# Kernel optimization log

Hardware: AMD Instinct MI355X
Metric: run time of the kernel (lower is better)

Reference implementation:

```python
import jax, jax.numpy as jnp
import numpy as np
from jax import lax

PATCH = 32  # enc conv kernel/stride
EPS = 1e-12  # F.normalize eps


def setup_inputs() -> dict:
    key = jax.random.key(0)
    ks = jax.random.split(key, 7)
    B, N, H, W = 32, 256, 32, 32
    fdim, vdim = 512, 128
    x = jax.random.normal(ks[0], (B, 3 * N, H, W), dtype=jnp.float32)
    conv_w = jax.random.normal(ks[1], (fdim, 3, PATCH, PATCH), dtype=jnp.float32) * (1.0 / np.sqrt(3 * PATCH * PATCH))
    conv_b = jax.random.normal(ks[2], (fdim,), dtype=jnp.float32) * 0.01
    fc1_w = jax.random.normal(ks[3], (vdim, fdim), dtype=jnp.float32) * (1.0 / np.sqrt(fdim))
    fc1_b = jax.random.normal(ks[4], (vdim,), dtype=jnp.float32) * 0.01
    # deterministic dropout masks (p=0.5, train mode -> keep * 1/(1-p))
    drop1 = (jax.random.uniform(ks[5], (B, N, N)) >= 0.5).astype(jnp.float32) * 2.0
    drop2 = (jax.random.uniform(ks[6], (B, N, N)) >= 0.5).astype(jnp.float32) * 2.0
    return {"x": x, "conv_w": conv_w, "conv_b": conv_b,
            "fc1_w": fc1_w, "fc1_b": fc1_b, "drop1": drop1, "drop2": drop2}


def _branch(scores, drop, eye):
    # softmax over dim=-2, zero diag, dropout, L1-normalize over dim=-2
    P = jax.nn.softmax(scores, axis=-2)
    P = P * (1.0 - eye)
    P = P * drop
    denom = jnp.maximum(jnp.sum(jnp.abs(P), axis=-2, keepdims=True), EPS)
    return P / denom


def reference(x, conv_w, conv_b, fc1_w, fc1_b, drop1, drop2):
    B, C, H, W = x.shape
    N = C // 3
    xi = x.reshape(B * N, 3, H, W)
    # enc: patchify conv -> (B*N, fdim, 1, 1)
    fm = lax.conv_general_dilated(xi, conv_w, (PATCH, PATCH), 'VALID',
                                  dimension_numbers=('NCHW', 'OIHW', 'NCHW'))
    fm = fm + conv_b[None, :, None, None]
    # map2vec: adaptive avgpool(1,1) + flatten + fc1
    v = fm.mean(axis=(2, 3))                      # (B*N, fdim)
    v = v @ fc1_w.T + fc1_b                       # (B*N, vdim)
    f = v.reshape(B, N, -1)                       # (B, N, vdim)
    f_norm = f / jnp.maximum(jnp.linalg.norm(f, axis=-1, keepdims=True), EPS)
    A = jnp.einsum('bnd,bmd->bnm', f_norm, f_norm)  # cosine affinity (B,N,N)
    Atemp = A * (128.0 ** 0.5)                    # torch.div(A, 1/128**0.5)
    eye = jnp.eye(N, dtype=A.dtype)
    A1 = _branch(Atemp, drop1, eye)
    A2t = _branch(jnp.swapaxes(Atemp, -1, -2), drop2, eye)
    AtA = jnp.swapaxes(jnp.matmul(A2t, A1), -1, -2)
    # nll_loss(AtA, arange targets) == -mean of diagonal entries
    diag = jnp.einsum('bii->bi', AtA)
    loss = -jnp.mean(diag)
    return f, A, loss
```

## Files before the change

kernel.cpp:

```cpp
#include <hip/hip_runtime.h>
#include <stdint.h>

#define S_SCALE 11.313708498984761f
#define EPS 1e-12f

typedef __bf16 bf16x8 __attribute__((ext_vector_type(8)));
typedef float  f32x4  __attribute__((ext_vector_type(4)));

__device__ __forceinline__ f32x4 mfma16(bf16x8 a, bf16x8 b, f32x4 c) {
  return __builtin_amdgcn_mfma_f32_16x16x32_bf16(a, b, c, 0, 0, 0);
}

__device__ __forceinline__ float waveSum(float v) {
#pragma unroll
  for (int m = 32; m > 0; m >>= 1) v += __shfl_xor(v, m, 64);
  return v;
}

__device__ __forceinline__ void load_lds16(const float* g, float* l) {
  __builtin_amdgcn_global_load_lds(
      (const __attribute__((address_space(1))) uint32_t*)g,
      (__attribute__((address_space(3))) uint32_t*)l, 16, 0, 0);
}

#define OFF_W    0
#define OFF_BIAS 786432
#define OFF_FN   786944
#define OFF_ZP   2884096
#define OFF_P1   3146240

__global__ __launch_bounds__(256) void k_prep(const float* __restrict__ conv_w,
                                              const float* __restrict__ fc1_w,
                                              const float* __restrict__ conv_b,
                                              const float* __restrict__ fc1_b,
                                              __bf16* __restrict__ W,
                                              float* __restrict__ bias2,
                                              float* __restrict__ loss) {
  __shared__ float cw_s[64][36];
  __shared__ float fc1_s[128][65];
  __shared__ float red[4];
  const int t = threadIdx.x;
  if (blockIdx.x >= 96) {
    const int o = blockIdx.x - 96;
    if (o == 0 && t == 0) loss[0] = 0.f;
    float p = fc1_w[o * 512 + t] * conv_b[t] +
              fc1_w[o * 512 + 256 + t] * conv_b[256 + t];
    p = waveSum(p);
    if ((t & 63) == 0) red[t >> 6] = p;
    __syncthreads();
    if (t == 0) bias2[o] = red[0] + red[1] + red[2] + red[3] + fc1_b[o];
    return;
  }
  const int kt = blockIdx.x;
  const int k0 = kt * 32;
  const int og = t >> 3, kg = t & 7;
  float acc[4][4] = {};
  for (int cs = 0; cs < 8; ++cs) {
    const int cc = cs * 64;
    __syncthreads();
#pragma unroll
    for (int i = 0; i < 8; ++i) {
      int idx = t + 256 * i;
      int cr = idx >> 5, kk = idx & 31;
      cw_s[cr][kk] = conv_w[(cc + cr) * 3072 + k0 + kk];
    }
#pragma unroll
    for (int i = 0; i < 8; ++i) {
      int idx = t + 256 * i;
      int o = idx >> 4, c4 = (idx & 15) * 4;
      float4 v = *(const float4*)&fc1_w[o * 512 + cc + c4];
      fc1_s[o][c4 + 0] = v.x; fc1_s[o][c4 + 1] = v.y;
      fc1_s[o][c4 + 2] = v.z; fc1_s[o][c4 + 3] = v.w;
    }
    __syncthreads();
    for (int ci = 0; ci < 64; ++ci) {
      float4 cw = *(const float4*)&cw_s[ci][kg * 4];
#pragma unroll
      for (int j = 0; j < 4; ++j) {
        float fv = fc1_s[og * 4 + j][ci];
        acc[j][0] = fmaf(fv, cw.x, acc[j][0]);
        acc[j][1] = fmaf(fv, cw.y, acc[j][1]);
        acc[j][2] = fmaf(fv, cw.z, acc[j][2]);
        acc[j][3] = fmaf(fv, cw.w, acc[j][3]);
      }
    }
  }
#pragma unroll
  for (int j = 0; j < 4; ++j)
#pragma unroll
    for (int q = 0; q < 4; ++q)
      W[(og * 4 + j) * 3072 + k0 + kg * 4 + q] = (__bf16)acc[j][q];
}

__device__ __forceinline__ void stageA(const float* __restrict__ x,
                                       float* __restrict__ lds, int wave,
                                       const int dr[2], const int dc[2],
                                       int m0, int k0) {
#pragma unroll
  for (int j = 0; j < 2; ++j)
    load_lds16(x + (m0 + dr[j]) * 3072 + k0 + dc[j],
               lds + (wave * 2 + j) * 256);
}

__device__ __forceinline__ void loadB(const __bf16* __restrict__ bp, int k0,
                                      uint4 (&dst)[2][2]) {
#pragma unroll
  for (int ks = 0; ks < 2; ++ks)
#pragma unroll
    for (int ni = 0; ni < 2; ++ni)
      dst[ks][ni] = *(const uint4*)(bp + ni * 16 * 3072 + k0 + ks * 32);
}

__device__ __forceinline__ void computeTile(const float* __restrict__ Abuf,
                                            const uint4 (&breg)[2][2],
                                            int l15, int quad,
                                            f32x4 (&acc)[2][2]) {
#pragma unroll
  for (int ks = 0; ks < 2; ++ks) {
    bf16x8 afrag[2];
#pragma unroll
    for (int mi = 0; mi < 2; ++mi) {
      const int rb = (l15 + mi * 16) * 64;
      float4 lo = *(const float4*)&Abuf[rb + (((ks * 8 + quad * 2 + 0) ^ l15) << 2)];
      float4 hi = *(const float4*)&Abuf[rb + (((ks * 8 + quad * 2 + 1) ^ l15) << 2)];
      union { __bf16 h[8]; bf16x8 v; } pk;
      pk.h[0] = (__bf16)lo.x; pk.h[1] = (__bf16)lo.y;
      pk.h[2] = (__bf16)lo.z; pk.h[3] = (__bf16)lo.w;
      pk.h[4] = (__bf16)hi.x; pk.h[5] = (__bf16)hi.y;
      pk.h[6] = (__bf16)hi.z; pk.h[7] = (__bf16)hi.w;
      afrag[mi] = pk.v;
    }
#pragma unroll
    for (int mi = 0; mi < 2; ++mi)
#pragma unroll
      for (int ni = 0; ni < 2; ++ni)
        acc[mi][ni] = mfma16(afrag[mi], *(const bf16x8*)&breg[ks][ni],
                             acc[mi][ni]);
  }
}

__global__ __launch_bounds__(256) void k_gemm1(const float* __restrict__ x,
                                               const __bf16* __restrict__ W,
                                               float* __restrict__ P0,
                                               float* __restrict__ P1) {
  __shared__ __align__(16) float A_lds[2][32 * 64];
  const int t = threadIdx.x;
  const int wave = t >> 6, lane = t & 63;
  const int l15 = lane & 15, quad = lane >> 4;
  const int m0 = blockIdx.x * 32;
  const int kbase = blockIdx.y * 1536;
  float* P = blockIdx.y ? P1 : P0;

  int dr[2], dc[2];
#pragma unroll
  for (int j = 0; j < 2; ++j) {
    int row = wave * 8 + j * 4 + (lane >> 4);
    int cl = (lane & 15) ^ (row & 15);
    dr[j] = row;
    dc[j] = cl * 4;
  }

  f32x4 acc[2][2] = {{{0.f,0.f,0.f,0.f},{0.f,0.f,0.f,0.f}},
                     {{0.f,0.f,0.f,0.f},{0.f,0.f,0.f,0.f}}};
  const __bf16* bp = W + (wave * 32 + l15) * 3072 + quad * 8;

  uint4 bA[2][2], bB[2][2];
  stageA(x, &A_lds[0][0], wave, dr, dc, m0, kbase);
  loadB(bp, kbase, bA);
  __syncthreads();

  for (int it2 = 0; it2 < 12; ++it2) {
    const int itA = it2 * 2;
    stageA(x, &A_lds[1][0], wave, dr, dc, m0, kbase + (itA + 1) * 64);
    loadB(bp, kbase + (itA + 1) * 64, bB);
    __builtin_amdgcn_sched_barrier(0);
    computeTile(&A_lds[0][0], bA, l15, quad, acc);
    __syncthreads();
    if (it2 < 11) {
      stageA(x, &A_lds[0][0], wave, dr, dc, m0, kbase + (itA + 2) * 64);
      loadB(bp, kbase + (itA + 2) * 64, bA);
    }
    __builtin_amdgcn_sched_barrier(0);
    computeTile(&A_lds[1][0], bB, l15, quad, acc);
    __syncthreads();
  }

#pragma unroll
  for (int mi = 0; mi < 2; ++mi)
#pragma unroll
    for (int ni = 0; ni < 2; ++ni) {
      int col = wave * 32 + ni * 16 + l15;
#pragma unroll
      for (int r = 0; r < 4; ++r) {
        int row = m0 + mi * 16 + quad * 4 + r;
        P[row * 128 + col] = acc[mi][ni][r];
      }
    }
}

__global__ __launch_bounds__(256) void k_fin(float* __restrict__ f_inout,
                                             const float* __restrict__ P1,
                                             const float* __restrict__ bias2,
                                             __bf16* __restrict__ fn) {
  const int wave = threadIdx.x >> 6, lane = threadIdx.x & 63;
  const int row = blockIdx.x * 4 + wave;
  const int i0 = row * 128 + lane, i1 = i0 + 64;
  float v0 = f_inout[i0] + P1[i0] + bias2[lane];
  float v1 = f_inout[i1] + P1[i1] + bias2[lane + 64];
  float ss = waveSum(fmaf(v0, v0, v1 * v1));
  float inv = 1.f / fmaxf(sqrtf(ss), EPS);
  f_inout[i0] = v0;
  f_inout[i1] = v1;
  fn[i0] = (__bf16)(v0 * inv);
  fn[i1] = (__bf16)(v1 * inv);
}

__global__ __launch_bounds__(256) void k_gemm2(const __bf16* __restrict__ fn,
                                               const float* __restrict__ d1,
                                               const float* __restrict__ d2,
                                               float* __restrict__ Aout,
                                               float* __restrict__ Zp) {
  __shared__ __align__(16) __bf16 Li[64][136];
  __shared__ __align__(16) __bf16 Lj[64][136];
  __shared__ float zred[2][4][64];
  const int t = threadIdx.x;
  const int b = blockIdx.y;
  const int ti = blockIdx.x >> 2, tj = blockIdx.x & 3;
  const int i0 = ti * 64, j0 = tj * 64;
  const int wave = t >> 6, lane = t & 63;
  const int l15 = lane & 15, quad = lane >> 4;
  const __bf16* fb = fn + b * 32768;
#pragma unroll
  for (int i = 0; i < 4; ++i) {
    int idx = t + 256 * i;
    int r = idx >> 4, c8 = (idx & 15) * 8;
    *(uint4*)&Li[r][c8] = *(const uint4*)&fb[(i0 + r) * 128 + c8];
    *(uint4*)&Lj[r][c8] = *(const uint4*)&fb[(j0 + r) * 128 + c8];
  }
  __syncthreads();
  f32x4 acc[4] = {{0.f, 0.f, 0.f, 0.f}, {0.f, 0.f, 0.f, 0.f},
                  {0.f, 0.f, 0.f, 0.f}, {0.f, 0.f, 0.f, 0.f}};
#pragma unroll
  for (int ks = 0; ks < 4; ++ks) {
    bf16x8 af = *(const bf16x8*)&Li[wave * 16 + l15][ks * 32 + quad * 8];
#pragma unroll
    for (int nt = 0; nt < 4; ++nt) {
      bf16x8 bf = *(const bf16x8*)&Lj[nt * 16 + l15][ks * 32 + quad * 8];
      acc[nt] = mfma16(af, bf, acc[nt]);
    }
  }
  const int base = b * 65536;
  float* Ab = Aout + base;
  float z1c[4] = {0.f, 0.f, 0.f, 0.f}, z2c[4] = {0.f, 0.f, 0.f, 0.f};
#pragma unroll
  for (int nt = 0; nt < 4; ++nt) {
    int gj = j0 + nt * 16 + l15;
#pragma unroll
    for (int r = 0; r < 4; ++r) {
      int gi = i0 + wave * 16 + quad * 4 + r;
      float a = acc[nt][r];
      Ab[gi * 256 + gj] = a;
      float e = __expf(fmaf(S_SCALE, a, -S_SCALE));
      if (gi != gj) {
        int idx = base + gi * 256 + gj;
        z1c[nt] = fmaf(e, d1[idx], z1c[nt]);
        z2c[nt] = fmaf(e, d2[idx], z2c[nt]);
      }
    }
  }
#pragma unroll
  for (int nt = 0; nt < 4; ++nt) {
    z1c[nt] += __shfl_xor(z1c[nt], 16, 64);
    z1c[nt] += __shfl_xor(z1c[nt], 32, 64);
    z2c[nt] += __shfl_xor(z2c[nt], 16, 64);
    z2c[nt] += __shfl_xor(z2c[nt], 32, 64);
  }
  if (quad == 0) {
#pragma unroll
    for (int nt = 0; nt < 4; ++nt) {
      zred[0][wave][nt * 16 + l15] = z1c[nt];
      zred[1][wave][nt * 16 + l15] = z2c[nt];
    }
  }
  __syncthreads();
  if (t < 128) {
    int z = t >> 6, c = t & 63;
    float s = zred[z][0][c] + zred[z][1][c] + zred[z][2][c] + zred[z][3][c];
    Zp[(z * 4 + ti) * 8192 + b * 256 + j0 + c] = s;
  }
}

__global__ __launch_bounds__(256) void k_loss(const float* __restrict__ Aout,
                                              const float* __restrict__ d1,
                                              const float* __restrict__ d2,
                                              const float* __restrict__ Zp,
                                              float* __restrict__ loss) {
  __shared__ float d1s[64][65];
  __shared__ float z1s[64], z2s[64];
  __shared__ float red[4];
  const int t = threadIdx.x;
  const int b = blockIdx.y;
  const int ic = blockIdx.x >> 2, kc = blockIdx.x & 3;
  const int i0 = ic * 64, k0 = kc * 64;
  const int base = b * 65536;
  if (t < 64) {
    float s = 0.f;
#pragma unroll
    for (int p = 0; p < 4; ++p) s += Zp[p * 8192 + b * 256 + i0 + t];
    z1s[t] = 1.f / fmaxf(s, EPS);
  } else if (t < 128) {
    float s = 0.f;
#pragma unroll
    for (int p = 0; p < 4; ++p) s += Zp[(4 + p) * 8192 + b * 256 + k0 + t - 64];
    z2s[t - 64] = 1.f / fmaxf(s, EPS);
  }
#pragma unroll
  for (int ii = 0; ii < 16; ++ii) {
    int idx = t + 256 * ii;
    int kr = idx >> 6, ci = idx & 63;
    d1s[kr][ci] = d1[base + (k0 + kr) * 256 + i0 + ci];
  }
  __syncthreads();
  const int kl = t & 63, ig = t >> 6;
  float inv2 = z2s[kl];
  float accv = 0.f;
  for (int ii = 0; ii < 16; ++ii) {
    int il = ig * 16 + ii;
    int idx = base + (i0 + il) * 256 + k0 + kl;
    float a = Aout[idx];
    float e = __expf(fmaf(2.f * S_SCALE, a, -2.f * S_SCALE));
    float v = e * d2[idx] * d1s[kl][il] * z1s[il] * inv2;
    if (i0 + il != k0 + kl) accv += v;
  }
  accv = waveSum(accv);
  if ((t & 63) == 0) red[t >> 6] = accv;
  __syncthreads();
  if (t == 0) {
    float tot = red[0] + red[1] + red[2] + red[3];
    atomicAdd(loss, tot * (-1.f / 8192.f));
  }
}

extern "C" void kernel_launch(void* const* d_in, const int* in_sizes, int n_in,
                              void* d_out, int out_size, void* d_ws,
                              size_t ws_size, hipStream_t stream) {
  const float* x = (const float*)d_in[0];
  const float* conv_w = (const float*)d_in[1];
  const float* conv_b = (const float*)d_in[2];
  const float* fc1_w = (const float*)d_in[3];
  const float* fc1_b = (const float*)d_in[4];
  const float* drop1 = (const float*)d_in[5];
  const float* drop2 = (const float*)d_in[6];
  char* ws = (char*)d_ws;
  __bf16* W = (__bf16*)(ws + OFF_W);
  float* bias2 = (float*)(ws + OFF_BIAS);
  __bf16* fn = (__bf16*)(ws + OFF_FN);
  float* Zp = (float*)(ws + OFF_ZP);
  float* P1 = (float*)(ws + OFF_P1);
  float* f = (float*)d_out;
  float* Aout = f + 1048576;
  float* loss = f + 3145728;

  k_prep<<<224, 256, 0, stream>>>(conv_w, fc1_w, conv_b, fc1_b, W, bias2, loss);
  k_gemm1<<<dim3(256, 2), 256, 0, stream>>>(x, W, f, P1);
  k_fin<<<2048, 256, 0, stream>>>(f, P1, bias2, fn);
  k_gemm2<<<dim3(16, 32), 256, 0, stream>>>(fn, drop1, drop2, Aout, Zp);
  k_loss<<<dim3(16, 32), 256, 0, stream>>>(Aout, drop1, drop2, Zp, loss);
}
```

Measured before the change: 237.2 us.

## Fuse all five stages into one cooperative persistent kernel with grid syncs

Merges prep, gemm1, finalize, gemm2 and loss into one cooperative kernel of 512 blocks. Grid-wide syncs separate the stages, and a shared-memory union lets every phase reuse the same LDS. The aim is to remove four kernel launches and their launch gaps. The cost is grid barrier overhead and a 2-blocks-per-CU occupancy bound, with the old multi-kernel path kept as a fallback if the cooperative launch fails.

```diff
diff --git a/kernel.cpp b/kernel.cpp
--- a/kernel.cpp
+++ b/kernel.cpp
@@ -1,5 +1,8 @@
 #include <hip/hip_runtime.h>
+#include <hip/hip_cooperative_groups.h>
 #include <stdint.h>
+
+namespace cg = cooperative_groups;
 
 #define S_SCALE 11.313708498984761f
 #define EPS 1e-12f
@@ -29,30 +32,37 @@
 #define OFF_ZP   2884096
 #define OFF_P1   3146240
 
-__global__ __launch_bounds__(256) void k_prep(const float* __restrict__ conv_w,
-                                              const float* __restrict__ fc1_w,
-                                              const float* __restrict__ conv_b,
-                                              const float* __restrict__ fc1_b,
-                                              __bf16* __restrict__ W,
-                                              float* __restrict__ bias2,
-                                              float* __restrict__ loss) {
-  __shared__ float cw_s[64][36];
-  __shared__ float fc1_s[128][65];
-  __shared__ float red[4];
+union __align__(16) SharedU {
+  struct { float cw_s[64][36]; float fc1_s[128][65]; float red[4]; } prep;
+  struct { float A[2][2048]; } g1;
+  struct { __bf16 Li[64][136]; __bf16 Lj[64][136]; float zred[2][4][64]; } g2;
+  struct { float d1s[64][65]; float z1s[64]; float z2s[64]; float red[4]; } loss;
+};
+
+__device__ __forceinline__ void phase_prep(SharedU& S, int bid,
+                                           const float* __restrict__ conv_w,
+                                           const float* __restrict__ fc1_w,
+                                           const float* __restrict__ conv_b,
+                                           const float* __restrict__ fc1_b,
+                                           __bf16* __restrict__ W,
+                                           float* __restrict__ bias2,
+                                           float* __restrict__ loss) {
   const int t = threadIdx.x;
-  if (blockIdx.x >= 96) {
-    const int o = blockIdx.x - 96;
+  if (bid >= 224) return;
+  if (bid >= 96) {
+    const int o = bid - 96;
     if (o == 0 && t == 0) loss[0] = 0.f;
     float p = fc1_w[o * 512 + t] * conv_b[t] +
               fc1_w[o * 512 + 256 + t] * conv_b[256 + t];
     p = waveSum(p);
-    if ((t & 63) == 0) red[t >> 6] = p;
+    if ((t & 63) == 0) S.prep.red[t >> 6] = p;
     __syncthreads();
-    if (t == 0) bias2[o] = red[0] + red[1] + red[2] + red[3] + fc1_b[o];
+    if (t == 0)
+      bias2[o] = S.prep.red[0] + S.prep.red[1] + S.prep.red[2] +
+                 S.prep.red[3] + fc1_b[o];
     return;
   }
-  const int kt = blockIdx.x;
-  const int k0 = kt * 32;
+  const int k0 = bid * 32;
   const int og = t >> 3, kg = t & 7;
   float acc[4][4] = {};
   for (int cs = 0; cs < 8; ++cs) {
@@ -62,22 +72,22 @@
     for (int i = 0; i < 8; ++i) {
       int idx = t + 256 * i;
       int cr = idx >> 5, kk = idx & 31;
-      cw_s[cr][kk] = conv_w[(cc + cr) * 3072 + k0 + kk];
+      S.prep.cw_s[cr][kk] = conv_w[(cc + cr) * 3072 + k0 + kk];
     }
 #pragma unroll
     for (int i = 0; i < 8; ++i) {
       int idx = t + 256 * i;
       int o = idx >> 4, c4 = (idx & 15) * 4;
       float4 v = *(const float4*)&fc1_w[o * 512 + cc + c4];
-      fc1_s[o][c4 + 0] = v.x; fc1_s[o][c4 + 1] = v.y;
-      fc1_s[o][c4 + 2] = v.z; fc1_s[o][c4 + 3] = v.w;
+      S.prep.fc1_s[o][c4 + 0] = v.x; S.prep.fc1_s[o][c4 + 1] = v.y;
+      S.prep.fc1_s[o][c4 + 2] = v.z; S.prep.fc1_s[o][c4 + 3] = v.w;
     }
     __syncthreads();
     for (int ci = 0; ci < 64; ++ci) {
-      float4 cw = *(const float4*)&cw_s[ci][kg * 4];
+      float4 cw = *(const float4*)&S.prep.cw_s[ci][kg * 4];
 #pragma unroll
       for (int j = 0; j < 4; ++j) {
-        float fv = fc1_s[og * 4 + j][ci];
+        float fv = S.prep.fc1_s[og * 4 + j][ci];
         acc[j][0] = fmaf(fv, cw.x, acc[j][0]);
         acc[j][1] = fmaf(fv, cw.y, acc[j][1]);
         acc[j][2] = fmaf(fv, cw.z, acc[j][2]);
@@ -139,17 +149,19 @@
   }
 }
 
-__global__ __launch_bounds__(256) void k_gemm1(const float* __restrict__ x,
-                                               const __bf16* __restrict__ W,
-                                               float* __restrict__ P0,
-                                               float* __restrict__ P1) {
-  __shared__ __align__(16) float A_lds[2][32 * 64];
+__device__ __forceinline__ void phase_gemm1(SharedU& S, int bid,
+                                            const float* __restrict__ x,
+                                            const __bf16* __restrict__ W,
+                                            float* __restrict__ P0,
+                                            float* __restrict__ P1) {
+  float* L0 = &S.g1.A[0][0];
+  float* L1 = &S.g1.A[1][0];
   const int t = threadIdx.x;
   const int wave = t >> 6, lane = t & 63;
   const int l15 = lane & 15, quad = lane >> 4;
-  const int m0 = blockIdx.x * 32;
-  const int kbase = blockIdx.y * 1536;
-  float* P = blockIdx.y ? P1 : P0;
+  const int m0 = (bid >> 1) * 32;
+  const int kbase = (bid & 1) * 1536;
+  float* P = (bid & 1) ? P1 : P0;
 
   int dr[2], dc[2];
 #pragma unroll
@@ -165,23 +177,23 @@
   const __bf16* bp = W + (wave * 32 + l15) * 3072 + quad * 8;
 
   uint4 bA[2][2], bB[2][2];
-  stageA(x, &A_lds[0][0], wave, dr, dc, m0, kbase);
+  stageA(x, L0, wave, dr, dc, m0, kbase);
   loadB(bp, kbase, bA);
   __syncthreads();
 
   for (int it2 = 0; it2 < 12; ++it2) {
     const int itA = it2 * 2;
-    stageA(x, &A_lds[1][0], wave, dr, dc, m0, kbase + (itA + 1) * 64);
+    stageA(x, L1, wave, dr, dc, m0, kbase + (itA + 1) * 64);
     loadB(bp, kbase + (itA + 1) * 64, bB);
     __builtin_amdgcn_sched_barrier(0);
-    computeTile(&A_lds[0][0], bA, l15, quad, acc);
+    computeTile(L0, bA, l15, quad, acc);
     __syncthreads();
     if (it2 < 11) {
-      stageA(x, &A_lds[0][0], wave, dr, dc, m0, kbase + (itA + 2) * 64);
+      stageA(x, L0, wave, dr, dc, m0, kbase + (itA + 2) * 64);
       loadB(bp, kbase + (itA + 2) * 64, bA);
     }
     __builtin_amdgcn_sched_barrier(0);
-    computeTile(&A_lds[1][0], bB, l15, quad, acc);
+    computeTile(L1, bB, l15, quad, acc);
     __syncthreads();
   }
 
@@ -198,34 +210,37 @@
     }
 }
 
-__global__ __launch_bounds__(256) void k_fin(float* __restrict__ f_inout,
-                                             const float* __restrict__ P1,
-                                             const float* __restrict__ bias2,
-                                             __bf16* __restrict__ fn) {
+__device__ __forceinline__ void phase_fin(int bid,
+                                          float* __restrict__ f_inout,
+                                          const float* __restrict__ P1,
+                                          const float* __restrict__ bias2,
+                                          __bf16* __restrict__ fn) {
   const int wave = threadIdx.x >> 6, lane = threadIdx.x & 63;
-  const int row = blockIdx.x * 4 + wave;
-  const int i0 = row * 128 + lane, i1 = i0 + 64;
-  float v0 = f_inout[i0] + P1[i0] + bias2[lane];
-  float v1 = f_inout[i1] + P1[i1] + bias2[lane + 64];
-  float ss = waveSum(fmaf(v0, v0, v1 * v1));
-  float inv = 1.f / fmaxf(sqrtf(ss), EPS);
-  f_inout[i0] = v0;
-  f_inout[i1] = v1;
-  fn[i0] = (__bf16)(v0 * inv);
-  fn[i1] = (__bf16)(v1 * inv);
-}
-
-__global__ __launch_bounds__(256) void k_gemm2(const __bf16* __restrict__ fn,
-                                               const float* __restrict__ d1,
-                                               const float* __restrict__ d2,
-                                               float* __restrict__ Aout,
-                                               float* __restrict__ Zp) {
-  __shared__ __align__(16) __bf16 Li[64][136];
-  __shared__ __align__(16) __bf16 Lj[64][136];
-  __shared__ float zred[2][4][64];
+#pragma unroll
+  for (int r = 0; r < 4; ++r) {
+    const int row = bid * 16 + r * 4 + wave;
+    const int i0 = row * 128 + lane, i1 = i0 + 64;
+    float v0 = f_inout[i0] + P1[i0] + bias2[lane];
+    float v1 = f_inout[i1] + P1[i1] + bias2[lane + 64];
+    float ss = waveSum(fmaf(v0, v0, v1 * v1));
+    float inv = 1.f / fmaxf(sqrtf(ss), EPS);
+    f_inout[i0] = v0;
+    f_inout[i1] = v1;
+    fn[i0] = (__bf16)(v0 * inv);
+    fn[i1] = (__bf16)(v1 * inv);
+  }
+}
+
+__device__ __forceinline__ void phase_gemm2(SharedU& S, int bid,
+                                            const __bf16* __restrict__ fn,
+                                            const float* __restrict__ d1,
+                                            const float* __restrict__ d2,
+                                            float* __restrict__ Aout,
+                                            float* __restrict__ Zp) {
   const int t = threadIdx.x;
-  const int b = blockIdx.y;
-  const int ti = blockIdx.x >> 2, tj = blockIdx.x & 3;
+  const int b = bid >> 4;
+  const int xx = bid & 15;
+  const int ti = xx >> 2, tj = xx & 3;
   const int i0 = ti * 64, j0 = tj * 64;
   const int wave = t >> 6, lane = t & 63;
   const int l15 = lane & 15, quad = lane >> 4;
@@ -234,18 +249,18 @@
   for (int i = 0; i < 4; ++i) {
     int idx = t + 256 * i;
     int r = idx >> 4, c8 = (idx & 15) * 8;
-    *(uint4*)&Li[r][c8] = *(const uint4*)&fb[(i0 + r) * 128 + c8];
-    *(uint4*)&Lj[r][c8] = *(const uint4*)&fb[(j0 + r) * 128 + c8];
+    *(uint4*)&S.g2.Li[r][c8] = *(const uint4*)&fb[(i0 + r) * 128 + c8];
+    *(uint4*)&S.g2.Lj[r][c8] = *(const uint4*)&fb[(j0 + r) * 128 + c8];
   }
   __syncthreads();
   f32x4 acc[4] = {{0.f, 0.f, 0.f, 0.f}, {0.f, 0.f, 0.f, 0.f},
                   {0.f, 0.f, 0.f, 0.f}, {0.f, 0.f, 0.f, 0.f}};
 #pragma unroll
   for (int ks = 0; ks < 4; ++ks) {
-    bf16x8 af = *(const bf16x8*)&Li[wave * 16 + l15][ks * 32 + quad * 8];
+    bf16x8 af = *(const bf16x8*)&S.g2.Li[wave * 16 + l15][ks * 32 + quad * 8];
 #pragma unroll
     for (int nt = 0; nt < 4; ++nt) {
-      bf16x8 bf = *(const bf16x8*)&Lj[nt * 16 + l15][ks * 32 + quad * 8];
+      bf16x8 bf = *(const bf16x8*)&S.g2.Lj[nt * 16 + l15][ks * 32 + quad * 8];
       acc[nt] = mfma16(af, bf, acc[nt]);
     }
   }
@@ -278,67 +293,123 @@
   if (quad == 0) {
 #pragma unroll
     for (int nt = 0; nt < 4; ++nt) {
-      zred[0][wave][nt * 16 + l15] = z1c[nt];
-      zred[1][wave][nt * 16 + l15] = z2c[nt];
+      S.g2.zred[0][wave][nt * 16 + l15] = z1c[nt];
+      S.g2.zred[1][wave][nt * 16 + l15] = z2c[nt];
     }
   }
   __syncthreads();
   if (t < 128) {
     int z = t >> 6, c = t & 63;
-    float s = zred[z][0][c] + zred[z][1][c] + zred[z][2][c] + zred[z][3][c];
+    float s = S.g2.zred[z][0][c] + S.g2.zred[z][1][c] +
+              S.g2.zred[z][2][c] + S.g2.zred[z][3][c];
     Zp[(z * 4 + ti) * 8192 + b * 256 + j0 + c] = s;
   }
 }
 
-__global__ __launch_bounds__(256) void k_loss(const float* __restrict__ Aout,
-                                              const float* __restrict__ d1,
-                                              const float* __restrict__ d2,
-                                              const float* __restrict__ Zp,
-                                              float* __restrict__ loss) {
-  __shared__ float d1s[64][65];
-  __shared__ float z1s[64], z2s[64];
-  __shared__ float red[4];
+__device__ __forceinline__ void phase_loss(SharedU& S, int bid,
+                                           const float* __restrict__ Aout,
+                                           const float* __restrict__ d1,
+                                           const float* __restrict__ d2,
+                                           const float* __restrict__ Zp,
+                                           float* __restrict__ loss) {
   const int t = threadIdx.x;
-  const int b = blockIdx.y;
-  const int ic = blockIdx.x >> 2, kc = blockIdx.x & 3;
+  const int b = bid >> 4;
+  const int xx = bid & 15;
+  const int ic = xx >> 2, kc = xx & 3;
   const int i0 = ic * 64, k0 = kc * 64;
   const int base = b * 65536;
   if (t < 64) {
     float s = 0.f;
 #pragma unroll
     for (int p = 0; p < 4; ++p) s += Zp[p * 8192 + b * 256 + i0 + t];
-    z1s[t] = 1.f / fmaxf(s, EPS);
+    S.loss.z1s[t] = 1.f / fmaxf(s, EPS);
   } else if (t < 128) {
     float s = 0.f;
 #pragma unroll
     for (int p = 0; p < 4; ++p) s += Zp[(4 + p) * 8192 + b * 256 + k0 + t - 64];
-    z2s[t - 64] = 1.f / fmaxf(s, EPS);
+    S.loss.z2s[t - 64] = 1.f / fmaxf(s, EPS);
   }
 #pragma unroll
   for (int ii = 0; ii < 16; ++ii) {
     int idx = t + 256 * ii;
     int kr = idx >> 6, ci = idx & 63;
-    d1s[kr][ci] = d1[base + (k0 + kr) * 256 + i0 + ci];
+    S.loss.d1s[kr][ci] = d1[base + (k0 + kr) * 256 + i0 + ci];
   }
   __syncthreads();
   const int kl = t & 63, ig = t >> 6;
-  float inv2 = z2s[kl];
+  float inv2 = S.loss.z2s[kl];
   float accv = 0.f;
   for (int ii = 0; ii < 16; ++ii) {
     int il = ig * 16 + ii;
     int idx = base + (i0 + il) * 256 + k0 + kl;
     float a = Aout[idx];
     float e = __expf(fmaf(2.f * S_SCALE, a, -2.f * S_SCALE));
-    float v = e * d2[idx] * d1s[kl][il] * z1s[il] * inv2;
+    float v = e * d2[idx] * S.loss.d1s[kl][il] * S.loss.z1s[il] * inv2;
     if (i0 + il != k0 + kl) accv += v;
   }
   accv = waveSum(accv);
-  if ((t & 63) == 0) red[t >> 6] = accv;
+  if ((t & 63) == 0) S.loss.red[t >> 6] = accv;
   __syncthreads();
   if (t == 0) {
-    float tot = red[0] + red[1] + red[2] + red[3];
+    float tot = S.loss.red[0] + S.loss.red[1] + S.loss.red[2] + S.loss.red[3];
     atomicAdd(loss, tot * (-1.f / 8192.f));
   }
+}
+
+__global__ __launch_bounds__(256, 2) void k_mega(
+    const float* __restrict__ x, const float* __restrict__ conv_w,
+    const float* __restrict__ conv_b, const float* __restrict__ fc1_w,
+    const float* __restrict__ fc1_b, const float* __restrict__ drop1,
+    const float* __restrict__ drop2, __bf16* __restrict__ W,
+    float* __restrict__ bias2, __bf16* __restrict__ fn,
+    float* __restrict__ Zp, float* __restrict__ P1, float* __restrict__ f,
+    float* __restrict__ Aout, float* __restrict__ loss) {
+  __shared__ SharedU S;
+  const int bid = blockIdx.x;
+  cg::grid_group g = cg::this_grid();
+  phase_prep(S, bid, conv_w, fc1_w, conv_b, fc1_b, W, bias2, loss);
+  g.sync();
+  phase_gemm1(S, bid, x, W, f, P1);
+  g.sync();
+  phase_fin(bid, f, P1, bias2, fn);
+  g.sync();
+  phase_gemm2(S, bid, fn, drop1, drop2, Aout, Zp);
+  g.sync();
+  phase_loss(S, bid, Aout, drop1, drop2, Zp, loss);
+}
+
+__global__ __launch_bounds__(256) void k_prep_s(const float* conv_w,
+                                                const float* fc1_w,
+                                                const float* conv_b,
+                                                const float* fc1_b, __bf16* W,
+                                                float* bias2, float* loss) {
+  __shared__ SharedU S;
+  phase_prep(S, blockIdx.x, conv_w, fc1_w, conv_b, fc1_b, W, bias2, loss);
+}
+__global__ __launch_bounds__(256) void k_gemm1_s(const float* x,
+                                                 const __bf16* W, float* P0,
+                                                 float* P1) {
+  __shared__ SharedU S;
+  phase_gemm1(S, blockIdx.x, x, W, P0, P1);
+}
+__global__ __launch_bounds__(256) void k_fin_s(float* f, const float* P1,
+                                               const float* bias2,
+                                               __bf16* fn) {
+  phase_fin(blockIdx.x, f, P1, bias2, fn);
+}
+__global__ __launch_bounds__(256) void k_gemm2_s(const __bf16* fn,
+                                                 const float* d1,
+                                                 const float* d2, float* Aout,
+                                                 float* Zp) {
+  __shared__ SharedU S;
+  phase_gemm2(S, blockIdx.x, fn, d1, d2, Aout, Zp);
+}
+__global__ __launch_bounds__(256) void k_loss_s(const float* Aout,
+                                                const float* d1,
+                                                const float* d2,
+                                                const float* Zp, float* loss) {
+  __shared__ SharedU S;
+  phase_loss(S, blockIdx.x, Aout, d1, d2, Zp, loss);
 }
 
 extern "C" void kernel_launch(void* const* d_in, const int* in_sizes, int n_in,
@@ -361,9 +432,19 @@
   float* Aout = f + 1048576;
   float* loss = f + 3145728;
 
-  k_prep<<<224, 256, 0, stream>>>(conv_w, fc1_w, conv_b, fc1_b, W, bias2, loss);
-  k_gemm1<<<dim3(256, 2), 256, 0, stream>>>(x, W, f, P1);
-  k_fin<<<2048, 256, 0, stream>>>(f, P1, bias2, fn);
-  k_gemm2<<<dim3(16, 32), 256, 0, stream>>>(fn, drop1, drop2, Aout, Zp);
-  k_loss<<<dim3(16, 32), 256, 0, stream>>>(Aout, drop1, drop2, Zp, loss);
-}
+  void* kargs[] = {(void*)&x,     (void*)&conv_w, (void*)&conv_b,
+                   (void*)&fc1_w, (void*)&fc1_b,  (void*)&drop1,
+                   (void*)&drop2, (void*)&W,      (void*)&bias2,
+                   (void*)&fn,    (void*)&Zp,     (void*)&P1,
+                   (void*)&f,     (void*)&Aout,   (void*)&loss};
+  hipError_t err = hipLaunchCooperativeKernel(
+      (const void*)k_mega, dim3(512), dim3(256), kargs, 0, stream);
+  if (err != hipSuccess) {
+    k_prep_s<<<224, 256, 0, stream>>>(conv_w, fc1_w, conv_b, fc1_b, W, bias2,
+                                      loss);
+    k_gemm1_s<<<512, 256, 0, stream>>>(x, W, f, P1);
+    k_fin_s<<<512, 256, 0, stream>>>(f, P1, bias2, fn);
+    k_gemm2_s<<<512, 256, 0, stream>>>(fn, drop1, drop2, Aout, Zp);
+    k_loss_s<<<512, 256, 0, stream>>>(Aout, drop1, drop2, Zp, loss);
+  }
+}
```

Measured after the change: 487.1 us. 105% more time.

## Fuse bias and row normalization into full-K GEMM1 and drop split-K pass

Applied to the files above, without the earlier changes.

GEMM1 now runs over the full K dimension with 16-row tiles and a 4-stage LDS ring buffer fed by direct global-to-LDS loads. Bias add and L2 normalization happen in its epilogue, which removes the P1 partial buffer and the separate k_fin kernel. k_prep is also split across twice as many blocks, each computing half of the output rows, to raise parallelism. In exchange each GEMM1 block performs a longer serial K loop, and each B (weight) fragment is reused across fewer rows.

```diff
diff --git a/kernel.cpp b/kernel.cpp
--- a/kernel.cpp
+++ b/kernel.cpp
@@ -27,7 +27,6 @@
 #define OFF_BIAS 786432
 #define OFF_FN   786944
 #define OFF_ZP   2884096
-#define OFF_P1   3146240
 
 __global__ __launch_bounds__(256) void k_prep(const float* __restrict__ conv_w,
                                               const float* __restrict__ fc1_w,
@@ -37,11 +36,11 @@
                                               float* __restrict__ bias2,
                                               float* __restrict__ loss) {
   __shared__ float cw_s[64][36];
-  __shared__ float fc1_s[128][65];
+  __shared__ float fc1_s[64][65];
   __shared__ float red[4];
   const int t = threadIdx.x;
-  if (blockIdx.x >= 96) {
-    const int o = blockIdx.x - 96;
+  if (blockIdx.x >= 192) {
+    const int o = blockIdx.x - 192;
     if (o == 0 && t == 0) loss[0] = 0.f;
     float p = fc1_w[o * 512 + t] * conv_b[t] +
               fc1_w[o * 512 + 256 + t] * conv_b[256 + t];
@@ -51,10 +50,11 @@
     if (t == 0) bias2[o] = red[0] + red[1] + red[2] + red[3] + fc1_b[o];
     return;
   }
-  const int kt = blockIdx.x;
-  const int k0 = kt * 32;
+  const int oh = blockIdx.x & 1;
+  const int kt = blockIdx.x >> 1;
+  const int k0 = kt * 32, o0 = oh * 64;
   const int og = t >> 3, kg = t & 7;
-  float acc[4][4] = {};
+  float acc[2][4] = {};
   for (int cs = 0; cs < 8; ++cs) {
     const int cc = cs * 64;
     __syncthreads();
@@ -65,10 +65,10 @@
       cw_s[cr][kk] = conv_w[(cc + cr) * 3072 + k0 + kk];
     }
 #pragma unroll
-    for (int i = 0; i < 8; ++i) {
+    for (int i = 0; i < 4; ++i) {
       int idx = t + 256 * i;
       int o = idx >> 4, c4 = (idx & 15) * 4;
-      float4 v = *(const float4*)&fc1_w[o * 512 + cc + c4];
+      float4 v = *(const float4*)&fc1_w[(o0 + o) * 512 + cc + c4];
       fc1_s[o][c4 + 0] = v.x; fc1_s[o][c4 + 1] = v.y;
       fc1_s[o][c4 + 2] = v.z; fc1_s[o][c4 + 3] = v.w;
     }
@@ -76,8 +76,8 @@
     for (int ci = 0; ci < 64; ++ci) {
       float4 cw = *(const float4*)&cw_s[ci][kg * 4];
 #pragma unroll
-      for (int j = 0; j < 4; ++j) {
-        float fv = fc1_s[og * 4 + j][ci];
+      for (int j = 0; j < 2; ++j) {
+        float fv = fc1_s[og * 2 + j][ci];
         acc[j][0] = fmaf(fv, cw.x, acc[j][0]);
         acc[j][1] = fmaf(fv, cw.y, acc[j][1]);
         acc[j][2] = fmaf(fv, cw.z, acc[j][2]);
@@ -86,20 +86,10 @@
     }
   }
 #pragma unroll
-  for (int j = 0; j < 4; ++j)
+  for (int j = 0; j < 2; ++j)
 #pragma unroll
     for (int q = 0; q < 4; ++q)
-      W[(og * 4 + j) * 3072 + k0 + kg * 4 + q] = (__bf16)acc[j][q];
-}
-
-__device__ __forceinline__ void stageA(const float* __restrict__ x,
-                                       float* __restrict__ lds, int wave,
-                                       const int dr[2], const int dc[2],
-                                       int m0, int k0) {
-#pragma unroll
-  for (int j = 0; j < 2; ++j)
-    load_lds16(x + (m0 + dr[j]) * 3072 + k0 + dc[j],
-               lds + (wave * 2 + j) * 256);
+      W[(o0 + og * 2 + j) * 3072 + k0 + kg * 4 + q] = (__bf16)acc[j][q];
 }
 
 __device__ __forceinline__ void loadB(const __bf16* __restrict__ bp, int k0,
@@ -111,108 +101,111 @@
       dst[ks][ni] = *(const uint4*)(bp + ni * 16 * 3072 + k0 + ks * 32);
 }
 
-__device__ __forceinline__ void computeTile(const float* __restrict__ Abuf,
-                                            const uint4 (&breg)[2][2],
-                                            int l15, int quad,
-                                            f32x4 (&acc)[2][2]) {
+__device__ __forceinline__ void computeTile16(const float* __restrict__ Abuf,
+                                              const uint4 (&breg)[2][2],
+                                              int l15, int quad,
+                                              f32x4 (&acc)[2]) {
+  const int rb = l15 * 64;
 #pragma unroll
   for (int ks = 0; ks < 2; ++ks) {
-    bf16x8 afrag[2];
-#pragma unroll
-    for (int mi = 0; mi < 2; ++mi) {
-      const int rb = (l15 + mi * 16) * 64;
-      float4 lo = *(const float4*)&Abuf[rb + (((ks * 8 + quad * 2 + 0) ^ l15) << 2)];
-      float4 hi = *(const float4*)&Abuf[rb + (((ks * 8 + quad * 2 + 1) ^ l15) << 2)];
-      union { __bf16 h[8]; bf16x8 v; } pk;
-      pk.h[0] = (__bf16)lo.x; pk.h[1] = (__bf16)lo.y;
-      pk.h[2] = (__bf16)lo.z; pk.h[3] = (__bf16)lo.w;
-      pk.h[4] = (__bf16)hi.x; pk.h[5] = (__bf16)hi.y;
-      pk.h[6] = (__bf16)hi.z; pk.h[7] = (__bf16)hi.w;
-      afrag[mi] = pk.v;
-    }
-#pragma unroll
-    for (int mi = 0; mi < 2; ++mi)
-#pragma unroll
-      for (int ni = 0; ni < 2; ++ni)
-        acc[mi][ni] = mfma16(afrag[mi], *(const bf16x8*)&breg[ks][ni],
-                             acc[mi][ni]);
-  }
-}
-
-__global__ __launch_bounds__(256) void k_gemm1(const float* __restrict__ x,
-                                               const __bf16* __restrict__ W,
-                                               float* __restrict__ P0,
-                                               float* __restrict__ P1) {
-  __shared__ __align__(16) float A_lds[2][32 * 64];
+    float4 lo = *(const float4*)&Abuf[rb + (((ks * 8 + quad * 2 + 0) ^ l15) << 2)];
+    float4 hi = *(const float4*)&Abuf[rb + (((ks * 8 + quad * 2 + 1) ^ l15) << 2)];
+    union { __bf16 h[8]; bf16x8 v; } pk;
+    pk.h[0] = (__bf16)lo.x; pk.h[1] = (__bf16)lo.y;
+    pk.h[2] = (__bf16)lo.z; pk.h[3] = (__bf16)lo.w;
+    pk.h[4] = (__bf16)hi.x; pk.h[5] = (__bf16)hi.y;
+    pk.h[6] = (__bf16)hi.z; pk.h[7] = (__bf16)hi.w;
+    bf16x8 af = pk.v;
+#pragma unroll
+    for (int ni = 0; ni < 2; ++ni)
+      acc[ni] = mfma16(af, *(const bf16x8*)&breg[ks][ni], acc[ni]);
+  }
+}
+
+__global__ __launch_bounds__(256) void k_gemm1f(const float* __restrict__ x,
+                                                const __bf16* __restrict__ W,
+                                                const float* __restrict__ bias2,
+                                                float* __restrict__ f,
+                                                __bf16* __restrict__ fn) {
+  __shared__ __align__(16) float A_lds[4][1024];
+  __shared__ float rsum[16][5];
+  __shared__ float rinv[16];
   const int t = threadIdx.x;
   const int wave = t >> 6, lane = t & 63;
   const int l15 = lane & 15, quad = lane >> 4;
-  const int m0 = blockIdx.x * 32;
-  const int kbase = blockIdx.y * 1536;
-  float* P = blockIdx.y ? P1 : P0;
-
-  int dr[2], dc[2];
-#pragma unroll
-  for (int j = 0; j < 2; ++j) {
-    int row = wave * 8 + j * 4 + (lane >> 4);
-    int cl = (lane & 15) ^ (row & 15);
-    dr[j] = row;
-    dc[j] = cl * 4;
-  }
-
-  f32x4 acc[2][2] = {{{0.f,0.f,0.f,0.f},{0.f,0.f,0.f,0.f}},
-                     {{0.f,0.f,0.f,0.f},{0.f,0.f,0.f,0.f}}};
+  const int m0 = blockIdx.x * 16;
+  const int dr = wave * 4 + (lane >> 4);
+  const int dc = ((lane & 15) ^ (dr & 15)) * 4;
+  const float* xrow = x + (m0 + dr) * 3072 + dc;
   const __bf16* bp = W + (wave * 32 + l15) * 3072 + quad * 8;
 
-  uint4 bA[2][2], bB[2][2];
-  stageA(x, &A_lds[0][0], wave, dr, dc, m0, kbase);
-  loadB(bp, kbase, bA);
-  __syncthreads();
-
-  for (int it2 = 0; it2 < 12; ++it2) {
-    const int itA = it2 * 2;
-    stageA(x, &A_lds[1][0], wave, dr, dc, m0, kbase + (itA + 1) * 64);
-    loadB(bp, kbase + (itA + 1) * 64, bB);
-    __builtin_amdgcn_sched_barrier(0);
-    computeTile(&A_lds[0][0], bA, l15, quad, acc);
-    __syncthreads();
-    if (it2 < 11) {
-      stageA(x, &A_lds[0][0], wave, dr, dc, m0, kbase + (itA + 2) * 64);
-      loadB(bp, kbase + (itA + 2) * 64, bA);
-    }
-    __builtin_amdgcn_sched_barrier(0);
-    computeTile(&A_lds[1][0], bB, l15, quad, acc);
-    __syncthreads();
-  }
-
-#pragma unroll
-  for (int mi = 0; mi < 2; ++mi)
-#pragma unroll
-    for (int ni = 0; ni < 2; ++ni) {
-      int col = wave * 32 + ni * 16 + l15;
-#pragma unroll
-      for (int r = 0; r < 4; ++r) {
-        int row = m0 + mi * 16 + quad * 4 + r;
-        P[row * 128 + col] = acc[mi][ni][r];
-      }
-    }
-}
-
-__global__ __launch_bounds__(256) void k_fin(float* __restrict__ f_inout,
-                                             const float* __restrict__ P1,
-                                             const float* __restrict__ bias2,
-                                             __bf16* __restrict__ fn) {
-  const int wave = threadIdx.x >> 6, lane = threadIdx.x & 63;
-  const int row = blockIdx.x * 4 + wave;
-  const int i0 = row * 128 + lane, i1 = i0 + 64;
-  float v0 = f_inout[i0] + P1[i0] + bias2[lane];
-  float v1 = f_inout[i1] + P1[i1] + bias2[lane + 64];
-  float ss = waveSum(fmaf(v0, v0, v1 * v1));
-  float inv = 1.f / fmaxf(sqrtf(ss), EPS);
-  f_inout[i0] = v0;
-  f_inout[i1] = v1;
-  fn[i0] = (__bf16)(v0 * inv);
-  fn[i1] = (__bf16)(v1 * inv);
+  f32x4 acc[2] = {{0.f, 0.f, 0.f, 0.f}, {0.f, 0.f, 0.f, 0.f}};
+  uint4 brA[2][2], brB[2][2];
+
+  loadB(bp, 0, brA);
+  load_lds16(xrow + 0 * 64, &A_lds[0][wave * 256]);
+  load_lds16(xrow + 1 * 64, &A_lds[1][wave * 256]);
+  load_lds16(xrow + 2 * 64, &A_lds[2][wave * 256]);
+
+  for (int it2 = 0; it2 < 24; ++it2) {
+    const int T0 = it2 * 2, T1 = T0 + 1;
+    asm volatile("s_waitcnt vmcnt(1)" ::: "memory");
+    __builtin_amdgcn_s_barrier();
+    __builtin_amdgcn_sched_barrier(0);
+    loadB(bp, (T0 + 1) * 64, brB);
+    __builtin_amdgcn_sched_barrier(0);
+    {
+      int dk = T0 + 3 > 47 ? 47 : T0 + 3;
+      load_lds16(xrow + dk * 64, &A_lds[(T0 + 3) & 3][wave * 256]);
+    }
+    __builtin_amdgcn_sched_barrier(0);
+    computeTile16(&A_lds[T0 & 3][0], brA, l15, quad, acc);
+    asm volatile("s_waitcnt vmcnt(1)" ::: "memory");
+    __builtin_amdgcn_s_barrier();
+    __builtin_amdgcn_sched_barrier(0);
+    {
+      int bk = T1 + 1 > 47 ? 47 : T1 + 1;
+      loadB(bp, bk * 64, brA);
+    }
+    __builtin_amdgcn_sched_barrier(0);
+    {
+      int dk = T1 + 3 > 47 ? 47 : T1 + 3;
+      load_lds16(xrow + dk * 64, &A_lds[(T1 + 3) & 3][wave * 256]);
+    }
+    __builtin_amdgcn_sched_barrier(0);
+    computeTile16(&A_lds[T1 & 3][0], brB, l15, quad, acc);
+  }
+
+  __syncthreads();
+  const float b0 = bias2[wave * 32 + l15];
+  const float b1 = bias2[wave * 32 + 16 + l15];
+#pragma unroll
+  for (int r = 0; r < 4; ++r) {
+    acc[0][r] += b0;
+    acc[1][r] += b1;
+    float s = acc[0][r] * acc[0][r] + acc[1][r] * acc[1][r];
+    s += __shfl_xor(s, 1, 64);
+    s += __shfl_xor(s, 2, 64);
+    s += __shfl_xor(s, 4, 64);
+    s += __shfl_xor(s, 8, 64);
+    if (l15 == 0) rsum[quad * 4 + r][wave] = s;
+  }
+  __syncthreads();
+  if (t < 16) {
+    float s = rsum[t][0] + rsum[t][1] + rsum[t][2] + rsum[t][3];
+    rinv[t] = 1.f / fmaxf(sqrtf(s), EPS);
+  }
+  __syncthreads();
+#pragma unroll
+  for (int r = 0; r < 4; ++r) {
+    const int row = quad * 4 + r;
+    const float iv = rinv[row];
+    const int g = (m0 + row) * 128 + wave * 32 + l15;
+    f[g] = acc[0][r];
+    fn[g] = (__bf16)(acc[0][r] * iv);
+    f[g + 16] = acc[1][r];
+    fn[g + 16] = (__bf16)(acc[1][r] * iv);
+  }
 }
 
 __global__ __launch_bounds__(256) void k_gemm2(const __bf16* __restrict__ fn,
@@ -356,14 +349,12 @@
   float* bias2 = (float*)(ws + OFF_BIAS);
   __bf16* fn = (__bf16*)(ws + OFF_FN);
   float* Zp = (float*)(ws + OFF_ZP);
-  float* P1 = (float*)(ws + OFF_P1);
   float* f = (float*)d_out;
   float* Aout = f + 1048576;
   float* loss = f + 3145728;
 
-  k_prep<<<224, 256, 0, stream>>>(conv_w, fc1_w, conv_b, fc1_b, W, bias2, loss);
-  k_gemm1<<<dim3(256, 2), 256, 0, stream>>>(x, W, f, P1);
-  k_fin<<<2048, 256, 0, stream>>>(f, P1, bias2, fn);
+  k_prep<<<320, 256, 0, stream>>>(conv_w, fc1_w, conv_b, fc1_b, W, bias2, loss);
+  k_gemm1f<<<512, 256, 0, stream>>>(x, W, bias2, f, fn);
   k_gemm2<<<dim3(16, 32), 256, 0, stream>>>(fn, drop1, drop2, Aout, Zp);
   k_loss<<<dim3(16, 32), 256, 0, stream>>>(Aout, drop1, drop2, Zp, loss);
 }
```

New measurement: 248.2 us. 4.6% more time.
